# Kernel optimization log

Measured on AMD Instinct MI355X. Metric: run time of the kernel, lower is better.

The kernel has to match this reference:

```python
import jax, jax.numpy as jnp
import numpy as np

def setup_inputs() -> dict:
    key = jax.random.key(0)
    QKV = jax.random.normal(key, (3, 2, 8, 4096, 64), dtype=jnp.float32)
    return {"QKV": QKV}

def reference(QKV):
    Q, K, V = QKV[0], QKV[1], QKV[2]            # each [B, H, N, d]
    scores = jnp.einsum('bhnd,bhmd->bhnm', Q, K)  # full N x N score matrix (no scaling, matching source)
    attn = jax.nn.softmax(scores, axis=-1)
    return jnp.einsum('bhnm,bhmd->bhnd', attn, V)
```

## Files before the change

### kernel.cpp

```cpp
#include <hip/hip_runtime.h>


typedef _Float16 f16x8 __attribute__((ext_vector_type(8)));
typedef _Float16 f16x4 __attribute__((ext_vector_type(4)));
typedef _Float16 f16x2 __attribute__((ext_vector_type(2)));
typedef short s16x8 __attribute__((ext_vector_type(8)));
typedef short s16x4 __attribute__((ext_vector_type(4)));
typedef float f32x4 __attribute__((ext_vector_type(4)));

#define NHEADS 16
#define SEQ 4096
#define HDIM 64
#define BR 128
#define BC 64
#define KP 72
#define PP 72
#define NSPLIT 2
#define MPAD 4.0f

__device__ __forceinline__ float fast_exp2(float x) {
#if __has_builtin(__builtin_amdgcn_exp2f)
  return __builtin_amdgcn_exp2f(x);
#else
  return exp2f(x);
#endif
}

__device__ __forceinline__ f16x2 pkrtz(float a, float b) {
  return __builtin_bit_cast(f16x2, __builtin_amdgcn_cvt_pkrtz(a, b));
}

__device__ __forceinline__ unsigned short f2bf(float f) {
  unsigned u = __builtin_bit_cast(unsigned, f);
  u += 0x7fffu + ((u >> 16) & 1u);
  return (unsigned short)(u >> 16);
}

__device__ __forceinline__ unsigned bfpack2(float a, float b) {
  return (__builtin_bit_cast(unsigned, b) & 0xffff0000u) |
         (__builtin_bit_cast(unsigned, a) >> 16);
}

__global__ __launch_bounds__(256) void conv_vt(const float* __restrict__ V,
                                               short* __restrict__ Vt) {
  const int bh = blockIdx.x >> 6;
  const int nt = blockIdx.x & 63;
  __shared__ __align__(16) short T[64 * KP];
  const float* Vh = V + (size_t)bh * SEQ * HDIM + (size_t)nt * 64 * HDIM;
  const int t = threadIdx.x;
  #pragma unroll
  for (int p = 0; p < 4; ++p) {
    int idx = t + p * 256;
    int row = idx >> 4, c4 = (idx & 15) << 2;
    float4 v = *(const float4*)(Vh + row * HDIM + c4);
    s16x4 h;
    h[0] = (short)f2bf(v.x); h[1] = (short)f2bf(v.y);
    h[2] = (short)f2bf(v.z); h[3] = (short)f2bf(v.w);
    *(s16x4*)&T[row * KP + c4] = h;
  }
  __syncthreads();
  const int d = t & 63, w = t >> 6;
  s16x8 o0, o1;
  #pragma unroll
  for (int j = 0; j < 8; ++j) o0[j] = T[(w * 16 + j) * KP + d];
  #pragma unroll
  for (int j = 0; j < 8; ++j) o1[j] = T[(w * 16 + 8 + j) * KP + d];
  short* out = Vt + (size_t)bh * HDIM * SEQ + (size_t)d * SEQ + nt * 64 + w * 16;
  *(s16x8*)out = o0;
  *(s16x8*)(out + 8) = o1;
}

__global__ __launch_bounds__(256) void combine2(const _Float16* __restrict__ Op,
                                                const float2* __restrict__ Ml,
                                                float* __restrict__ O) {
  const size_t tensElems = (size_t)NHEADS * SEQ * HDIM;
  size_t t = (size_t)blockIdx.x * 256 + threadIdx.x;
  size_t row = t >> 3;
  int seg = (int)(t & 7) << 3;
  float2 s0 = Ml[row];
  float2 s1 = Ml[(size_t)NHEADS * SEQ + row];
  float Ms = fmaxf(s0.x, s1.x);
  float a0 = fast_exp2(s0.x - Ms) * s0.y;
  float a1 = fast_exp2(s1.x - Ms) * s1.y;
  float inv = 1.0f / (a0 + a1);
  a0 *= inv;
  a1 *= inv;
  f16x8 o0 = *(const f16x8*)(Op + row * HDIM + seg);
  f16x8 o1 = *(const f16x8*)(Op + tensElems + row * HDIM + seg);
  float4 r0, r1;
  r0.x = (float)o0[0] * a0 + (float)o1[0] * a1;
  r0.y = (float)o0[1] * a0 + (float)o1[1] * a1;
  r0.z = (float)o0[2] * a0 + (float)o1[2] * a1;
  r0.w = (float)o0[3] * a0 + (float)o1[3] * a1;
  r1.x = (float)o0[4] * a0 + (float)o1[4] * a1;
  r1.y = (float)o0[5] * a0 + (float)o1[5] * a1;
  r1.z = (float)o0[6] * a0 + (float)o1[6] * a1;
  r1.w = (float)o0[7] * a0 + (float)o1[7] * a1;
  *(float4*)(O + row * HDIM + seg) = r0;
  *(float4*)(O + row * HDIM + seg + 4) = r1;
}

template <bool PRE, bool SPLIT>
__global__ __launch_bounds__(256, 4) void flash_attn(const float* __restrict__ QKV,
                                                     const short* __restrict__ Vt16,
                                                     float* __restrict__ Out,
                                                     _Float16* __restrict__ Opart,
                                                     float2* __restrict__ Ml) {
  const size_t headElems = (size_t)SEQ * HDIM;
  const size_t tensElems = (size_t)NHEADS * headElems;
  const int bh = blockIdx.x & 15;
  const int qt = blockIdx.x >> 4;
  const int split = SPLIT ? blockIdx.y : 0;
  const int ktBeg = SPLIT ? split * (SEQ / BC / NSPLIT) : 0;
  const int ktN = SPLIT ? (SEQ / BC / NSPLIT) : (SEQ / BC);

  const float* Q = QKV + (size_t)bh * headElems;
  const float* Kf = QKV + tensElems + (size_t)bh * headElems;
  const float* Vf = QKV + 2 * tensElems + (size_t)bh * headElems;
  const short* Vg16 = Vt16 + (size_t)bh * headElems;
  float* O = Out + (size_t)bh * headElems;

  const int tid = threadIdx.x;
  const int wave = tid >> 6;
  const int lane = tid & 63;
  const int g = lane >> 4;
  const int l16 = lane & 15;

  __shared__ __align__(16) _Float16 Ks[BC * KP];
  __shared__ __align__(16) short Vs[HDIM * KP];
  __shared__ __align__(16) short Ps[4][2][16 * PP];

  const float LOG2E = 1.4426950408889634f;
  const int qbase = qt * BR + wave * 32;
  f16x8 qf[2][2];
  #pragma unroll
  for (int h = 0; h < 2; ++h) {
    const float* qp = Q + (size_t)(qbase + h * 16 + l16) * HDIM + g * 8;
    #pragma unroll
    for (int c = 0; c < 2; ++c) {
      float4 a = *(const float4*)(qp + c * 32);
      float4 b = *(const float4*)(qp + c * 32 + 4);
      union { f16x8 v; f16x2 h2[4]; } u;
      u.h2[0] = pkrtz(a.x * LOG2E, a.y * LOG2E);
      u.h2[1] = pkrtz(a.z * LOG2E, a.w * LOG2E);
      u.h2[2] = pkrtz(b.x * LOG2E, b.y * LOG2E);
      u.h2[3] = pkrtz(b.z * LOG2E, b.w * LOG2E);
      qf[h][c] = u.v;
    }
  }

  const int sr = tid >> 2;
  const int sc = (tid & 3) << 4;

  float4 kpre[4];
  s16x8 vpre[2];

  auto prefetch = [&](int kt) {
    if constexpr (PRE) {
      const float* kg = Kf + (size_t)(kt * BC + sr) * HDIM + sc;
      kpre[0] = *(const float4*)(kg);
      kpre[1] = *(const float4*)(kg + 4);
      kpre[2] = *(const float4*)(kg + 8);
      kpre[3] = *(const float4*)(kg + 12);
      const short* vg = Vg16 + (size_t)sr * SEQ + kt * BC + sc;
      vpre[0] = *(const s16x8*)(vg);
      vpre[1] = *(const s16x8*)(vg + 8);
    }
  };
  auto commit = [&](int kt) {
    if constexpr (PRE) {
      union { f16x8 v; f16x2 h2[4]; } ka, kb;
      ka.h2[0] = pkrtz(kpre[0].x, kpre[0].y);
      ka.h2[1] = pkrtz(kpre[0].z, kpre[0].w);
      ka.h2[2] = pkrtz(kpre[1].x, kpre[1].y);
      ka.h2[3] = pkrtz(kpre[1].z, kpre[1].w);
      kb.h2[0] = pkrtz(kpre[2].x, kpre[2].y);
      kb.h2[1] = pkrtz(kpre[2].z, kpre[2].w);
      kb.h2[2] = pkrtz(kpre[3].x, kpre[3].y);
      kb.h2[3] = pkrtz(kpre[3].z, kpre[3].w);
      *(f16x8*)&Ks[sr * KP + sc] = ka.v;
      *(f16x8*)&Ks[sr * KP + sc + 8] = kb.v;
      *(s16x8*)&Vs[sr * KP + sc] = vpre[0];
      *(s16x8*)&Vs[sr * KP + sc + 8] = vpre[1];
    } else {
      const float* kg = Kf + (size_t)(kt * BC + sr) * HDIM + sc;
      float4 a = *(const float4*)(kg), b = *(const float4*)(kg + 4);
      float4 c = *(const float4*)(kg + 8), d = *(const float4*)(kg + 12);
      union { f16x8 v; f16x2 h2[4]; } ka, kb;
      ka.h2[0] = pkrtz(a.x, a.y);
      ka.h2[1] = pkrtz(a.z, a.w);
      ka.h2[2] = pkrtz(b.x, b.y);
      ka.h2[3] = pkrtz(b.z, b.w);
      kb.h2[0] = pkrtz(c.x, c.y);
      kb.h2[1] = pkrtz(c.z, c.w);
      kb.h2[2] = pkrtz(d.x, d.y);
      kb.h2[3] = pkrtz(d.z, d.w);
      *(f16x8*)&Ks[sr * KP + sc] = ka.v;
      *(f16x8*)&Ks[sr * KP + sc + 8] = kb.v;
      const float* vg = Vf + (size_t)(kt * BC + sr) * HDIM + sc;
      float4 va = *(const float4*)(vg), vb = *(const float4*)(vg + 4);
      float4 vc = *(const float4*)(vg + 8), vd = *(const float4*)(vg + 12);
      float vv[16] = {va.x, va.y, va.z, va.w, vb.x, vb.y, vb.z, vb.w,
                      vc.x, vc.y, vc.z, vc.w, vd.x, vd.y, vd.z, vd.w};
      #pragma unroll
      for (int j = 0; j < 16; ++j) Vs[(sc + j) * KP + sr] = (short)f2bf(vv[j]);
    }
  };

  f32x4 acc[2][4];
  #pragma unroll
  for (int h = 0; h < 2; ++h)
    #pragma unroll
    for (int nt = 0; nt < 4; ++nt)
      #pragma unroll
      for (int i = 0; i < 4; ++i) acc[h][nt][i] = 0.f;
  float l_[2] = {0.f, 0.f};
  float negM[2] = {0.f, 0.f};

  prefetch(ktBeg);
  commit(ktBeg);

  for (int it = 0; it < ktN; ++it) {
    const int kt = ktBeg + it;
    __syncthreads();
    if (it < ktN - 1) prefetch(kt + 1);

    f32x4 s[2][4];
    #pragma unroll
    for (int jt = 0; jt < 4; ++jt) {
      const int ka = (jt * 16 + l16) * KP + g * 8;
      f16x8 k0 = *(const f16x8*)&Ks[ka];
      f16x8 k1 = *(const f16x8*)&Ks[ka + 32];
      #pragma unroll
      for (int h = 0; h < 2; ++h) {
        f32x4 z;
        z[0] = z[1] = z[2] = z[3] = negM[h];
        z = __builtin_amdgcn_mfma_f32_16x16x32_f16(k0, qf[h][0], z, 0, 0, 0);
        z = __builtin_amdgcn_mfma_f32_16x16x32_f16(k1, qf[h][1], z, 0, 0, 0);
        s[h][jt] = z;
      }
    }

    if (it == 0) {
      #pragma unroll
      for (int h = 0; h < 2; ++h) {
        float mx = s[h][0][0];
        #pragma unroll
        for (int jt = 0; jt < 4; ++jt)
          #pragma unroll
          for (int ri = 0; ri < 4; ++ri) mx = fmaxf(mx, s[h][jt][ri]);
        mx = fmaxf(mx, __shfl_xor(mx, 16));
        mx = fmaxf(mx, __shfl_xor(mx, 32));
        negM[h] = -(mx + MPAD);
        #pragma unroll
        for (int jt = 0; jt < 4; ++jt)
          #pragma unroll
          for (int ri = 0; ri < 4; ++ri) s[h][jt][ri] += negM[h];
      }
    }

    #pragma unroll
    for (int h = 0; h < 2; ++h) {
      float psum = l_[h];
      const int e0 = l16 * PP + 4 * g;
      #pragma unroll
      for (int jt = 0; jt < 4; ++jt) {
        float p0 = fast_exp2(s[h][jt][0]);
        float p1 = fast_exp2(s[h][jt][1]);
        float p2 = fast_exp2(s[h][jt][2]);
        float p3 = fast_exp2(s[h][jt][3]);
        psum += (p0 + p1) + (p2 + p3);
        uint2 w;
        w.x = bfpack2(p0, p1);
        w.y = bfpack2(p2, p3);
        *(uint2*)&Ps[wave][h][e0 + jt * 16] = w;
      }
      l_[h] = psum;
    }

    s16x8 pa[2][2];
    #pragma unroll
    for (int h = 0; h < 2; ++h) {
      pa[h][0] = *(const s16x8*)&Ps[wave][h][l16 * PP + g * 8];
      pa[h][1] = *(const s16x8*)&Ps[wave][h][l16 * PP + g * 8 + 32];
    }
    #pragma unroll
    for (int nt = 0; nt < 4; ++nt) {
      const int va = (nt * 16 + l16) * KP + g * 8;
      s16x8 v0 = *(const s16x8*)&Vs[va];
      s16x8 v1 = *(const s16x8*)&Vs[va + 32];
      #pragma unroll
      for (int h = 0; h < 2; ++h) {
        acc[h][nt] = __builtin_amdgcn_mfma_f32_16x16x32_bf16(pa[h][0], v0, acc[h][nt], 0, 0, 0);
        acc[h][nt] = __builtin_amdgcn_mfma_f32_16x16x32_bf16(pa[h][1], v1, acc[h][nt], 0, 0, 0);
      }
    }

    __syncthreads();
    if (it < ktN - 1) commit(kt + 1);
  }

  #pragma unroll
  for (int h = 0; h < 2; ++h) {
    float lf = l_[h];
    lf += __shfl_xor(lf, 16);
    lf += __shfl_xor(lf, 32);
    float linv = 1.0f / lf;
    if constexpr (SPLIT) {
      if (g == 0) {
        Ml[(size_t)split * NHEADS * SEQ + (size_t)bh * SEQ + qbase + h * 16 + l16] =
            float2{-negM[h], lf};
      }
      _Float16* op = Opart + (size_t)split * tensElems + (size_t)bh * headElems;
      #pragma unroll
      for (int ri = 0; ri < 4; ++ri) {
        float lB = __shfl(linv, 4 * g + ri);
        const int row = qbase + h * 16 + 4 * g + ri;
        #pragma unroll
        for (int nt = 0; nt < 4; ++nt)
          op[(size_t)row * HDIM + nt * 16 + l16] = (_Float16)(acc[h][nt][ri] * lB);
      }
    } else {
      #pragma unroll
      for (int ri = 0; ri < 4; ++ri) {
        float lB = __shfl(linv, 4 * g + ri);
        const int row = qbase + h * 16 + 4 * g + ri;
        #pragma unroll
        for (int nt = 0; nt < 4; ++nt)
          O[(size_t)row * HDIM + nt * 16 + l16] = acc[h][nt][ri] * lB;
      }
    }
  }
}

extern "C" void kernel_launch(void* const* d_in, const int* in_sizes, int n_in,
                              void* d_out, int out_size, void* d_ws, size_t ws_size,
                              hipStream_t stream) {
  const float* QKV = (const float*)d_in[0];
  float* Out = (float*)d_out;
  const size_t tensElems = (size_t)NHEADS * SEQ * HDIM;
  const size_t vtBytes = tensElems * sizeof(short);
  const size_t opBytes = (size_t)NSPLIT * tensElems * sizeof(_Float16);
  const size_t mlBytes = (size_t)NSPLIT * NHEADS * SEQ * 8;

  dim3 block(256);

  if (ws_size >= vtBytes + opBytes + mlBytes) {
    short* Vt16 = (short*)d_ws;
    _Float16* Opart = (_Float16*)((char*)d_ws + vtBytes);
    float2* Ml = (float2*)((char*)d_ws + vtBytes + opBytes);
    const float* V = QKV + 2 * tensElems;
    hipLaunchKernelGGL(conv_vt, dim3(NHEADS * (SEQ / 64)), block, 0, stream, V, Vt16);
    hipLaunchKernelGGL((flash_attn<true, true>), dim3(NHEADS * (SEQ / BR), NSPLIT),
                       block, 0, stream, QKV, Vt16, Out, Opart, Ml);
    hipLaunchKernelGGL(combine2, dim3((NHEADS * SEQ * HDIM / 8) / 256), block, 0,
                       stream, Opart, Ml, Out);
  } else if (ws_size >= vtBytes) {
    short* Vt16 = (short*)d_ws;
    const float* V = QKV + 2 * tensElems;
    hipLaunchKernelGGL(conv_vt, dim3(NHEADS * (SEQ / 64)), block, 0, stream, V, Vt16);
    hipLaunchKernelGGL((flash_attn<true, false>), dim3(NHEADS * (SEQ / BR)), block,
                       0, stream, QKV, Vt16, Out, (_Float16*)nullptr, (float2*)nullptr);
  } else {
    hipLaunchKernelGGL((flash_attn<false, false>), dim3(NHEADS * (SEQ / BR)), block,
                       0, stream, QKV, (const short*)nullptr, Out,
                       (_Float16*)nullptr, (float2*)nullptr);
  }
}
```

Measured before the change: 186.4 us.

## Double query tile per block and pre-convert K to fp16 in prep kernel

Raises the query tile from 128 to 256 rows (four 16-row groups per wave), so each K/V tile loaded into shared memory is reused across twice as many queries. A fused prep kernel now converts K to fp16 once, alongside the V bf16 transpose, so the attention kernel loads half-width K with no per-block conversion. The cost is more registers per wave (launch bounds lowered to 2 blocks), half as many blocks (grid of 512 with split 2), and extra workspace plus a global pass over K.

```diff
diff --git a/kernel.cpp b/kernel.cpp
--- a/kernel.cpp
+++ b/kernel.cpp
@@ -2,7 +2,6 @@
 
 
 typedef _Float16 f16x8 __attribute__((ext_vector_type(8)));
-typedef _Float16 f16x4 __attribute__((ext_vector_type(4)));
 typedef _Float16 f16x2 __attribute__((ext_vector_type(2)));
 typedef short s16x8 __attribute__((ext_vector_type(8)));
 typedef short s16x4 __attribute__((ext_vector_type(4)));
@@ -11,7 +10,8 @@
 #define NHEADS 16
 #define SEQ 4096
 #define HDIM 64
-#define BR 128
+#define BR 256
+#define NH 4
 #define BC 64
 #define KP 72
 #define PP 72
@@ -41,33 +41,50 @@
          (__builtin_bit_cast(unsigned, a) >> 16);
 }
 
-__global__ __launch_bounds__(256) void conv_vt(const float* __restrict__ V,
-                                               short* __restrict__ Vt) {
-  const int bh = blockIdx.x >> 6;
-  const int nt = blockIdx.x & 63;
+__global__ __launch_bounds__(256) void prep(const float* __restrict__ QKV,
+                                            _Float16* __restrict__ K16,
+                                            short* __restrict__ Vt) {
+  const size_t tensElems = (size_t)NHEADS * SEQ * HDIM;
   __shared__ __align__(16) short T[64 * KP];
-  const float* Vh = V + (size_t)bh * SEQ * HDIM + (size_t)nt * 64 * HDIM;
-  const int t = threadIdx.x;
-  #pragma unroll
-  for (int p = 0; p < 4; ++p) {
-    int idx = t + p * 256;
-    int row = idx >> 4, c4 = (idx & 15) << 2;
-    float4 v = *(const float4*)(Vh + row * HDIM + c4);
-    s16x4 h;
-    h[0] = (short)f2bf(v.x); h[1] = (short)f2bf(v.y);
-    h[2] = (short)f2bf(v.z); h[3] = (short)f2bf(v.w);
-    *(s16x4*)&T[row * KP + c4] = h;
-  }
-  __syncthreads();
-  const int d = t & 63, w = t >> 6;
-  s16x8 o0, o1;
-  #pragma unroll
-  for (int j = 0; j < 8; ++j) o0[j] = T[(w * 16 + j) * KP + d];
-  #pragma unroll
-  for (int j = 0; j < 8; ++j) o1[j] = T[(w * 16 + 8 + j) * KP + d];
-  short* out = Vt + (size_t)bh * HDIM * SEQ + (size_t)d * SEQ + nt * 64 + w * 16;
-  *(s16x8*)out = o0;
-  *(s16x8*)(out + 8) = o1;
+  if (blockIdx.x < 2048) {
+    const float* Kf = QKV + tensElems;
+    size_t i = ((size_t)blockIdx.x * 256 + threadIdx.x) * 8;
+    float4 a = *(const float4*)(Kf + i);
+    float4 b = *(const float4*)(Kf + i + 4);
+    union { f16x8 v; f16x2 h2[4]; } u;
+    u.h2[0] = pkrtz(a.x, a.y);
+    u.h2[1] = pkrtz(a.z, a.w);
+    u.h2[2] = pkrtz(b.x, b.y);
+    u.h2[3] = pkrtz(b.z, b.w);
+    *(f16x8*)(K16 + i) = u.v;
+  } else {
+    const int vb = blockIdx.x - 2048;
+    const int bh = vb >> 6;
+    const int nt = vb & 63;
+    const float* Vh = QKV + 2 * tensElems + (size_t)bh * SEQ * HDIM +
+                      (size_t)nt * 64 * HDIM;
+    const int t = threadIdx.x;
+    #pragma unroll
+    for (int p = 0; p < 4; ++p) {
+      int idx = t + p * 256;
+      int row = idx >> 4, c4 = (idx & 15) << 2;
+      float4 v = *(const float4*)(Vh + row * HDIM + c4);
+      s16x4 h;
+      h[0] = (short)f2bf(v.x); h[1] = (short)f2bf(v.y);
+      h[2] = (short)f2bf(v.z); h[3] = (short)f2bf(v.w);
+      *(s16x4*)&T[row * KP + c4] = h;
+    }
+    __syncthreads();
+    const int d = t & 63, w = t >> 6;
+    s16x8 o0, o1;
+    #pragma unroll
+    for (int j = 0; j < 8; ++j) o0[j] = T[(w * 16 + j) * KP + d];
+    #pragma unroll
+    for (int j = 0; j < 8; ++j) o1[j] = T[(w * 16 + 8 + j) * KP + d];
+    short* out = Vt + (size_t)bh * HDIM * SEQ + (size_t)d * SEQ + nt * 64 + w * 16;
+    *(s16x8*)out = o0;
+    *(s16x8*)(out + 8) = o1;
+  }
 }
 
 __global__ __launch_bounds__(256) void combine2(const _Float16* __restrict__ Op,
@@ -101,7 +118,8 @@
 }
 
 template <bool PRE, bool SPLIT>
-__global__ __launch_bounds__(256, 4) void flash_attn(const float* __restrict__ QKV,
+__global__ __launch_bounds__(256, 2) void flash_attn(const float* __restrict__ QKV,
+                                                     const _Float16* __restrict__ K16g,
                                                      const short* __restrict__ Vt16,
                                                      float* __restrict__ Out,
                                                      _Float16* __restrict__ Opart,
@@ -117,6 +135,7 @@
   const float* Q = QKV + (size_t)bh * headElems;
   const float* Kf = QKV + tensElems + (size_t)bh * headElems;
   const float* Vf = QKV + 2 * tensElems + (size_t)bh * headElems;
+  const _Float16* Kg16 = K16g + (size_t)bh * headElems;
   const short* Vg16 = Vt16 + (size_t)bh * headElems;
   float* O = Out + (size_t)bh * headElems;
 
@@ -128,13 +147,13 @@
 
   __shared__ __align__(16) _Float16 Ks[BC * KP];
   __shared__ __align__(16) short Vs[HDIM * KP];
-  __shared__ __align__(16) short Ps[4][2][16 * PP];
+  __shared__ __align__(16) short Ps[4][NH][16 * PP];
 
   const float LOG2E = 1.4426950408889634f;
-  const int qbase = qt * BR + wave * 32;
-  f16x8 qf[2][2];
+  const int qbase = qt * BR + wave * (16 * NH);
+  f16x8 qf[NH][2];
   #pragma unroll
-  for (int h = 0; h < 2; ++h) {
+  for (int h = 0; h < NH; ++h) {
     const float* qp = Q + (size_t)(qbase + h * 16 + l16) * HDIM + g * 8;
     #pragma unroll
     for (int c = 0; c < 2; ++c) {
@@ -152,16 +171,14 @@
   const int sr = tid >> 2;
   const int sc = (tid & 3) << 4;
 
-  float4 kpre[4];
+  s16x8 kpre[2];
   s16x8 vpre[2];
 
   auto prefetch = [&](int kt) {
     if constexpr (PRE) {
-      const float* kg = Kf + (size_t)(kt * BC + sr) * HDIM + sc;
-      kpre[0] = *(const float4*)(kg);
-      kpre[1] = *(const float4*)(kg + 4);
-      kpre[2] = *(const float4*)(kg + 8);
-      kpre[3] = *(const float4*)(kg + 12);
+      const _Float16* kg = Kg16 + (size_t)(kt * BC + sr) * HDIM + sc;
+      kpre[0] = *(const s16x8*)(kg);
+      kpre[1] = *(const s16x8*)(kg + 8);
       const short* vg = Vg16 + (size_t)sr * SEQ + kt * BC + sc;
       vpre[0] = *(const s16x8*)(vg);
       vpre[1] = *(const s16x8*)(vg + 8);
@@ -169,17 +186,8 @@
   };
   auto commit = [&](int kt) {
     if constexpr (PRE) {
-      union { f16x8 v; f16x2 h2[4]; } ka, kb;
-      ka.h2[0] = pkrtz(kpre[0].x, kpre[0].y);
-      ka.h2[1] = pkrtz(kpre[0].z, kpre[0].w);
-      ka.h2[2] = pkrtz(kpre[1].x, kpre[1].y);
-      ka.h2[3] = pkrtz(kpre[1].z, kpre[1].w);
-      kb.h2[0] = pkrtz(kpre[2].x, kpre[2].y);
-      kb.h2[1] = pkrtz(kpre[2].z, kpre[2].w);
-      kb.h2[2] = pkrtz(kpre[3].x, kpre[3].y);
-      kb.h2[3] = pkrtz(kpre[3].z, kpre[3].w);
-      *(f16x8*)&Ks[sr * KP + sc] = ka.v;
-      *(f16x8*)&Ks[sr * KP + sc + 8] = kb.v;
+      *(s16x8*)&Ks[sr * KP + sc] = kpre[0];
+      *(s16x8*)&Ks[sr * KP + sc + 8] = kpre[1];
       *(s16x8*)&Vs[sr * KP + sc] = vpre[0];
       *(s16x8*)&Vs[sr * KP + sc + 8] = vpre[1];
     } else {
@@ -207,15 +215,15 @@
     }
   };
 
-  f32x4 acc[2][4];
+  f32x4 acc[NH][4];
   #pragma unroll
-  for (int h = 0; h < 2; ++h)
+  for (int h = 0; h < NH; ++h)
     #pragma unroll
     for (int nt = 0; nt < 4; ++nt)
       #pragma unroll
       for (int i = 0; i < 4; ++i) acc[h][nt][i] = 0.f;
-  float l_[2] = {0.f, 0.f};
-  float negM[2] = {0.f, 0.f};
+  float l_[NH] = {0.f, 0.f, 0.f, 0.f};
+  float negM[NH] = {0.f, 0.f, 0.f, 0.f};
 
   prefetch(ktBeg);
   commit(ktBeg);
@@ -225,14 +233,14 @@
     __syncthreads();
     if (it < ktN - 1) prefetch(kt + 1);
 
-    f32x4 s[2][4];
+    f32x4 s[NH][4];
     #pragma unroll
     for (int jt = 0; jt < 4; ++jt) {
       const int ka = (jt * 16 + l16) * KP + g * 8;
       f16x8 k0 = *(const f16x8*)&Ks[ka];
       f16x8 k1 = *(const f16x8*)&Ks[ka + 32];
       #pragma unroll
-      for (int h = 0; h < 2; ++h) {
+      for (int h = 0; h < NH; ++h) {
         f32x4 z;
         z[0] = z[1] = z[2] = z[3] = negM[h];
         z = __builtin_amdgcn_mfma_f32_16x16x32_f16(k0, qf[h][0], z, 0, 0, 0);
@@ -243,7 +251,7 @@
 
     if (it == 0) {
       #pragma unroll
-      for (int h = 0; h < 2; ++h) {
+      for (int h = 0; h < NH; ++h) {
         float mx = s[h][0][0];
         #pragma unroll
         for (int jt = 0; jt < 4; ++jt)
@@ -260,7 +268,7 @@
     }
 
     #pragma unroll
-    for (int h = 0; h < 2; ++h) {
+    for (int h = 0; h < NH; ++h) {
       float psum = l_[h];
       const int e0 = l16 * PP + 4 * g;
       #pragma unroll
@@ -278,9 +286,9 @@
       l_[h] = psum;
     }
 
-    s16x8 pa[2][2];
-    #pragma unroll
-    for (int h = 0; h < 2; ++h) {
+    s16x8 pa[NH][2];
+    #pragma unroll
+    for (int h = 0; h < NH; ++h) {
       pa[h][0] = *(const s16x8*)&Ps[wave][h][l16 * PP + g * 8];
       pa[h][1] = *(const s16x8*)&Ps[wave][h][l16 * PP + g * 8 + 32];
     }
@@ -290,7 +298,7 @@
       s16x8 v0 = *(const s16x8*)&Vs[va];
       s16x8 v1 = *(const s16x8*)&Vs[va + 32];
       #pragma unroll
-      for (int h = 0; h < 2; ++h) {
+      for (int h = 0; h < NH; ++h) {
         acc[h][nt] = __builtin_amdgcn_mfma_f32_16x16x32_bf16(pa[h][0], v0, acc[h][nt], 0, 0, 0);
         acc[h][nt] = __builtin_amdgcn_mfma_f32_16x16x32_bf16(pa[h][1], v1, acc[h][nt], 0, 0, 0);
       }
@@ -301,7 +309,7 @@
   }
 
   #pragma unroll
-  for (int h = 0; h < 2; ++h) {
+  for (int h = 0; h < NH; ++h) {
     float lf = l_[h];
     lf += __shfl_xor(lf, 16);
     lf += __shfl_xor(lf, 32);
@@ -339,31 +347,27 @@
   const float* QKV = (const float*)d_in[0];
   float* Out = (float*)d_out;
   const size_t tensElems = (size_t)NHEADS * SEQ * HDIM;
+  const size_t k16Bytes = tensElems * sizeof(_Float16);
   const size_t vtBytes = tensElems * sizeof(short);
   const size_t opBytes = (size_t)NSPLIT * tensElems * sizeof(_Float16);
   const size_t mlBytes = (size_t)NSPLIT * NHEADS * SEQ * 8;
 
   dim3 block(256);
 
-  if (ws_size >= vtBytes + opBytes + mlBytes) {
-    short* Vt16 = (short*)d_ws;
-    _Float16* Opart = (_Float16*)((char*)d_ws + vtBytes);
-    float2* Ml = (float2*)((char*)d_ws + vtBytes + opBytes);
-    const float* V = QKV + 2 * tensElems;
-    hipLaunchKernelGGL(conv_vt, dim3(NHEADS * (SEQ / 64)), block, 0, stream, V, Vt16);
+  if (ws_size >= k16Bytes + vtBytes + opBytes + mlBytes) {
+    _Float16* K16 = (_Float16*)d_ws;
+    short* Vt16 = (short*)((char*)d_ws + k16Bytes);
+    _Float16* Opart = (_Float16*)((char*)d_ws + k16Bytes + vtBytes);
+    float2* Ml = (float2*)((char*)d_ws + k16Bytes + vtBytes + opBytes);
+    hipLaunchKernelGGL(prep, dim3(3072), block, 0, stream, QKV, K16, Vt16);
     hipLaunchKernelGGL((flash_attn<true, true>), dim3(NHEADS * (SEQ / BR), NSPLIT),
-                       block, 0, stream, QKV, Vt16, Out, Opart, Ml);
+                       block, 0, stream, QKV, K16, Vt16, Out, Opart, Ml);
     hipLaunchKernelGGL(combine2, dim3((NHEADS * SEQ * HDIM / 8) / 256), block, 0,
                        stream, Opart, Ml, Out);
-  } else if (ws_size >= vtBytes) {
-    short* Vt16 = (short*)d_ws;
-    const float* V = QKV + 2 * tensElems;
-    hipLaunchKernelGGL(conv_vt, dim3(NHEADS * (SEQ / 64)), block, 0, stream, V, Vt16);
-    hipLaunchKernelGGL((flash_attn<true, false>), dim3(NHEADS * (SEQ / BR)), block,
-                       0, stream, QKV, Vt16, Out, (_Float16*)nullptr, (float2*)nullptr);
   } else {
     hipLaunchKernelGGL((flash_attn<false, false>), dim3(NHEADS * (SEQ / BR)), block,
-                       0, stream, QKV, (const short*)nullptr, Out,
-                       (_Float16*)nullptr, (float2*)nullptr);
-  }
-}
+                       0, stream, QKV, (const _Float16*)nullptr,
+                       (const short*)nullptr, Out, (_Float16*)nullptr,
+                       (float2*)nullptr);
+  }
+}
```

New measurement: 170.7 us. 8.4% less time.
